# Performance work log

Measured on AMD Instinct MI355X. Metric: run time of the kernel, lower is better.

The kernel has to match this reference:

```python
import jax, jax.numpy as jnp
import numpy as np

B, S, D = 4, 2048, 1024

def setup_inputs() -> dict:
    key = jax.random.key(0)
    k1, k2, k3, k4 = jax.random.split(key, 4)
    scale = 1.0 / np.sqrt(D)
    x = jax.random.normal(k1, (B, S, D), dtype=jnp.float32)
    Wq = jax.random.normal(k2, (D, D), dtype=jnp.float32) * scale
    Wk = jax.random.normal(k3, (D, D), dtype=jnp.float32) * scale
    Wv = jax.random.normal(k4, (D, D), dtype=jnp.float32) * scale
    return {"x": x, "Wq": Wq, "Wk": Wk, "Wv": Wv}

def reference(x, Wq, Wk, Wv):
    # Linear projections (nn.Linear with bias=False computes x @ W.T)
    q = jnp.einsum('bsd,ed->bse', x, Wq)
    k = jnp.einsum('bsd,ed->bse', x, Wk)
    v = jnp.einsum('bsd,ed->bse', x, Wv)
    # HRR binding: circular convolution of k and v == elementwise product in FFT domain
    fq = jnp.fft.fft(q, axis=-1)
    fk = jnp.fft.fft(k, axis=-1)
    fv = jnp.fft.fft(v, axis=-1)
    # Causal associative memory: cumulative sum of bound key-value pairs over sequence
    mem = jnp.cumsum(fk * fv, axis=-2)  # [B, S, D] complex
    # Unbind with query via approximate inverse (complex conjugate of fft(q))
    out = jnp.fft.ifft(mem * jnp.conj(fq), axis=-1).real
    return out.astype(x.dtype)
```

## Files before the change

### kernel.cpp

```cpp
#include <hip/hip_runtime.h>

#define BB 4
#define SS 2048
#define DD 1024
#define MM 8192
#define CH 64
#define RR 32
#define PI_F 3.14159265358979323846f

typedef __attribute__((ext_vector_type(8))) short bf16x8;
typedef __attribute__((ext_vector_type(4))) float f32x4;

__device__ __forceinline__ unsigned short f2bf(float f) {
  unsigned int u = __float_as_uint(f);
  u = (u + 0x7FFFu + ((u >> 16) & 1u)) >> 16;
  return (unsigned short)u;
}
__device__ __forceinline__ float bf2f(unsigned short h) {
  return __uint_as_float(((unsigned int)h) << 16);
}

__global__ __launch_bounds__(256) void convert_bf16(
    const float* __restrict__ src, unsigned short* __restrict__ dst) {
  const long i = ((long)blockIdx.x * 256 + threadIdx.x) * 4;
  const float4 v = *(const float4*)&src[i];
  ushort4 o;
  o.x = f2bf(v.x); o.y = f2bf(v.y); o.z = f2bf(v.z); o.w = f2bf(v.w);
  *(ushort4*)&dst[i] = o;
}

__global__ __launch_bounds__(256) void convert_w(
    const float* __restrict__ Wq, const float* __restrict__ Wk,
    const float* __restrict__ Wv, unsigned short* __restrict__ dst) {
  const int z = blockIdx.y;
  const float* src = (z == 0) ? Wq : (z == 1) ? Wk : Wv;
  const long i = ((long)blockIdx.x * 256 + threadIdx.x) * 4;
  const float4 v = *(const float4*)&src[i];
  ushort4 o;
  o.x = f2bf(v.x); o.y = f2bf(v.y); o.z = f2bf(v.z); o.w = f2bf(v.w);
  *(ushort4*)&dst[(size_t)z * DD * DD + i] = o;
}

__device__ __forceinline__ void async16(const void* g, void* l) {
  __builtin_amdgcn_global_load_lds(
      (const __attribute__((address_space(1))) void*)g,
      (__attribute__((address_space(3))) void*)l, 16, 0, 0);
}

#define GW(n)  asm volatile("s_waitcnt vmcnt(" #n ")" ::: "memory")
#define BAR()  asm volatile("s_barrier" ::: "memory")
#define SB0()  __builtin_amdgcn_sched_barrier(0)

#define STA(buf, i, T) async16(xb + (size_t)(m0 + 32 * (i)) * DD + (T) * 64 + sOff, \
                               &Als[(buf) * 8192 + (i) * 2048 + slot8])
#define STB(buf, i, T) async16(W + (size_t)(n0 + 32 * (i)) * DD + (T) * 64 + sOff, \
                               &Bls[(buf) * 8192 + (i) * 2048 + slot8])
#define LDA(buf) { _Pragma("unroll") for (int mt = 0; mt < 4; ++mt) { \
    af[mt][0] = *(const bf16x8*)&Als[(buf) * 8192 + aRd + mt * 1024 + qoff0]; \
    af[mt][1] = *(const bf16x8*)&Als[(buf) * 8192 + aRd + mt * 1024 + qoff1]; } }
#define LDB(buf, nt, bank) { \
    bank[0] = *(const bf16x8*)&Bls[(buf) * 8192 + bRd + (nt) * 1024 + qoff0]; \
    bank[1] = *(const bf16x8*)&Bls[(buf) * 8192 + bRd + (nt) * 1024 + qoff1]; }
#define MMA(nt, bank) { __builtin_amdgcn_s_setprio(1); \
    _Pragma("unroll") for (int mt = 0; mt < 4; ++mt) { \
      acc[mt][nt] = __builtin_amdgcn_mfma_f32_16x16x32_bf16(af[mt][0], bank[0], acc[mt][nt], 0, 0, 0); \
      acc[mt][nt] = __builtin_amdgcn_mfma_f32_16x16x32_bf16(af[mt][1], bank[1], acc[mt][nt], 0, 0, 0); } \
    __builtin_amdgcn_s_setprio(0); }

__global__ __launch_bounds__(256, 2) void gemm_mfma(
    const unsigned short* __restrict__ xb,
    const unsigned short* __restrict__ Wb,
    float* __restrict__ outq, unsigned short* __restrict__ KV) {
  const int z = blockIdx.z;
  const unsigned short* W = Wb + (size_t)z * DD * DD;

  __shared__ unsigned short Als[2 * 8192];
  __shared__ unsigned short Bls[2 * 8192];

  const int tid  = threadIdx.x;
  const int lane = tid & 63;
  const int w    = tid >> 6;
  const int wm   = w >> 1;
  const int wn   = w & 1;
  const int fr   = lane & 15;
  const int kq   = lane >> 4;

  const int m0 = blockIdx.x * 128;
  const int n0 = blockIdx.y * 128;

  const int srow  = tid >> 3;
  const int sq    = (tid & 7) ^ (srow & 7);
  const int slot8 = tid * 8;
  const size_t sOff = (size_t)srow * DD + sq * 8;

  const int qoff0 = ((0 + kq) ^ (fr & 7)) * 8;
  const int qoff1 = ((4 + kq) ^ (fr & 7)) * 8;
  const int aRd = wm * 4096 + fr * 64;
  const int bRd = wn * 4096 + fr * 64;

  f32x4 acc[4][4] = {};
  bf16x8 af[4][2];
  bf16x8 bva[2], bvb[2];

  STA(0, 0, 0); STA(0, 1, 0); STA(0, 2, 0); STA(0, 3, 0);
  STB(0, 0, 0); STB(0, 1, 0); STB(0, 2, 0); STB(0, 3, 0);
  STA(1, 0, 1); STA(1, 1, 1); STA(1, 2, 1); STA(1, 3, 1);

  for (int T = 0; T < 14; ++T) {
    const int buf = T & 1;
    SB0(); GW(4); BAR();
    LDB(buf, 0, bva);
    LDA(buf);
    LDB(buf, 1, bvb);
    STB(buf ^ 1, 0, T + 1); STB(buf ^ 1, 1, T + 1);
    STB(buf ^ 1, 2, T + 1); STB(buf ^ 1, 3, T + 1);
    MMA(0, bva);
    MMA(1, bvb);
    SB0(); BAR();
    LDB(buf, 2, bva);
    LDB(buf, 3, bvb);
    STA(buf, 0, T + 2); STA(buf, 1, T + 2);
    STA(buf, 2, T + 2); STA(buf, 3, T + 2);
    MMA(2, bva);
    MMA(3, bvb);
  }
  SB0(); GW(4); BAR();
  LDB(0, 0, bva); LDA(0); LDB(0, 1, bvb);
  STB(1, 0, 15); STB(1, 1, 15); STB(1, 2, 15); STB(1, 3, 15);
  MMA(0, bva); MMA(1, bvb);
  SB0(); BAR();
  LDB(0, 2, bva); LDB(0, 3, bvb);
  MMA(2, bva); MMA(3, bvb);
  SB0(); GW(0); BAR();
  LDB(1, 0, bva); LDA(1); LDB(1, 1, bvb);
  MMA(0, bva); MMA(1, bvb);
  SB0(); BAR();
  LDB(1, 2, bva); LDB(1, 3, bvb);
  MMA(2, bva); MMA(3, bvb);

  const int col = lane & 15;
  const int r0  = (lane >> 4) * 4;
  const int mBase = m0 + wm * 64;
  const int nBase = n0 + wn * 64;
  if (z == 0) {
    #pragma unroll
    for (int mt = 0; mt < 4; ++mt)
      #pragma unroll
      for (int nt = 0; nt < 4; ++nt)
        #pragma unroll
        for (int r = 0; r < 4; ++r)
          outq[(size_t)(mBase + mt * 16 + r0 + r) * DD + nBase + nt * 16 + col] =
              acc[mt][nt][r];
  } else {
    unsigned short* Ck = KV + (size_t)(z - 1) * DD;
    #pragma unroll
    for (int mt = 0; mt < 4; ++mt)
      #pragma unroll
      for (int nt = 0; nt < 4; ++nt)
        #pragma unroll
        for (int r = 0; r < 4; ++r)
          Ck[(size_t)(mBase + mt * 16 + r0 + r) * 2048 + nBase + nt * 16 + col] =
              f2bf(acc[mt][nt][r]);
  }
}

__device__ __forceinline__ int pidx(int i) { return i + (i >> 6); }
#define BUFSZ 1040
__device__ __forceinline__ int pidx16(int i) { return i + (i >> 4); }
#define MEMSZ 546

__device__ __forceinline__ int rev4(int p) {
  unsigned r = __brev((unsigned)p) >> 22;
  return (int)(((r & 0x155u) << 1) | ((r & 0x2AAu) >> 1));
}

__host__ __device__ constexpr int clog2(int s) {
  return (s == 256) ? 8 : (s == 64) ? 6 : (s == 16) ? 4 : (s == 4) ? 2 : 0;
}

__device__ __forceinline__ void bf4(float2& a, float2& b, float2& c, float2& d,
                                    float c1, float s1) {
  const float c2 = c1 * c1 - s1 * s1, s2 = 2.0f * c1 * s1;
  const float c3 = c1 * c2 - s1 * s2, s3 = c1 * s2 + s1 * c2;
  const float Ar = a.x + c.x, Ai = a.y + c.y;
  const float Br = b.x + d.x, Bi = b.y + d.y;
  const float Cr = a.x - c.x, Ci = a.y - c.y;
  const float dr = b.x - d.x, di = b.y - d.y;
  const float y1r = Cr + di, y1i = Ci - dr;
  const float y2r = Ar - Br, y2i = Ai - Bi;
  const float y3r = Cr - di, y3i = Ci + dr;
  a = make_float2(Ar + Br, Ai + Bi);
  b = make_float2(y1r * c1 - y1i * s1, y1r * s1 + y1i * c1);
  c = make_float2(y2r * c2 - y2i * s2, y2r * s2 + y2i * c2);
  d = make_float2(y3r * c3 - y3i * s3, y3r * s3 + y3i * c3);
}

template <int S>
__device__ __forceinline__ void fwd_stage(float2 x[4], int t) {
  float c1 = 1.0f, s1 = 0.0f;
  if (S > 1) {
    const int j = t & (S - 1);
    __sincosf(-2.0f * PI_F * (float)j / (float)(4 * S), &s1, &c1);
  }
  bf4(x[0], x[1], x[2], x[3], c1, s1);
}

template <int S>
__device__ __forceinline__ void inv_stage(float2 x[4], int t) {
  float c1 = 1.0f, s1 = 0.0f;
  if (S > 1) {
    const int j = t & (S - 1);
    __sincosf(2.0f * PI_F * (float)j / (float)(4 * S), &s1, &c1);
  }
  const float c2 = c1 * c1 - s1 * s1, s2 = 2.0f * c1 * s1;
  const float c3 = c1 * c2 - s1 * s2, s3 = c1 * s2 + s1 * c2;
  const float u0r = x[0].x,                   u0i = x[0].y;
  const float u1r = x[1].x * c1 - x[1].y * s1, u1i = x[1].x * s1 + x[1].y * c1;
  const float u2r = x[2].x * c2 - x[2].y * s2, u2i = x[2].x * s2 + x[2].y * c2;
  const float u3r = x[3].x * c3 - x[3].y * s3, u3i = x[3].x * s3 + x[3].y * c3;
  const float Er = u0r + u2r, Ei = u0i + u2i;
  const float Fr = u0r - u2r, Fi = u0i - u2i;
  const float Gr = u1r + u3r, Gi = u1i + u3i;
  const float Hr = u1r - u3r, Hi = u1i - u3i;
  x[0] = make_float2(Er + Gr, Ei + Gi);
  x[1] = make_float2(Fr - Hi, Fi + Hr);
  x[2] = make_float2(Er - Gr, Ei - Gi);
  x[3] = make_float2(Fr + Hi, Fi - Hr);
}

template <int SW, int SR>
__device__ __forceinline__ void xchg(float2* buf, float2 x[4], int t) {
  constexpr int LW2 = clog2(SW), LR = clog2(SR);
  #pragma unroll
  for (int n = 0; n < 4; ++n)
    buf[pidx(((t >> LW2) << (LW2 + 2)) + (t & (SW - 1)) + n * SW)] = x[n];
  __syncthreads();
  #pragma unroll
  for (int n = 0; n < 4; ++n)
    x[n] = buf[pidx(((t >> LR) << (LR + 2)) + (t & (SR - 1)) + n * SR)];
  __syncthreads();
}

__device__ __forceinline__ void fwd_fft(float2* buf, float2 x[4], int t) {
  fwd_stage<256>(x, t); xchg<256, 64>(buf, x, t);
  fwd_stage<64>(x, t);  xchg<64, 16>(buf, x, t);
  fwd_stage<16>(x, t);  xchg<16, 4>(buf, x, t);
  fwd_stage<4>(x, t);   xchg<4, 1>(buf, x, t);
  fwd_stage<1>(x, t);
  #pragma unroll
  for (int n = 0; n < 4; ++n) buf[pidx(4 * t + n)] = x[n];
  __syncthreads();
}

#define LKW() asm volatile("s_waitcnt lgkmcnt(0)" ::: "memory")

__global__ __launch_bounds__(256) void bind_kernel(unsigned short* __restrict__ KV) {
  __shared__ float2 rbufs[4][BUFSZ];
  const int l  = threadIdx.x & 63;
  const int wv = threadIdx.x >> 6;
  float2* rbuf = rbufs[wv];
  unsigned short* row = KV + ((long)blockIdx.x * 4 + wv) * 2048;

  float2 x[16];
  #pragma unroll
  for (int j = 0; j < 16; ++j) {
    const int n = l + 64 * j;
    x[j] = make_float2(bf2f(row[n]), bf2f(row[1024 + n]));
  }

  #pragma unroll
  for (int b = 0; b < 4; ++b) {
    float s1, c1;
    __sincosf(-2.0f * PI_F * (float)(l + 64 * b) / 1024.0f, &s1, &c1);
    bf4(x[b], x[b + 4], x[b + 8], x[b + 12], c1, s1);
  }
  {
    float s1, c1;
    __sincosf(-2.0f * PI_F * (float)l / 256.0f, &s1, &c1);
    #pragma unroll
    for (int b = 0; b < 4; ++b)
      bf4(x[4 * b], x[4 * b + 1], x[4 * b + 2], x[4 * b + 3], c1, s1);
  }

  #pragma unroll
  for (int j = 0; j < 16; ++j)
    rbuf[(l ^ ((j & 3) << 2)) + 64 * j] = x[j];
  LKW();
  const int g = l >> 2, cc = l & 3;
  #pragma unroll
  for (int j = 0; j < 16; ++j) {
    const int q = 64 * g + cc + 4 * j;
    x[j] = rbuf[q ^ (((q >> 6) & 3) << 2)];
  }

  #pragma unroll
  for (int b = 0; b < 4; ++b) {
    float s1, c1;
    __sincosf(-2.0f * PI_F * (float)(cc + 4 * b) / 64.0f, &s1, &c1);
    bf4(x[b], x[b + 4], x[b + 8], x[b + 12], c1, s1);
  }
  {
    float s1, c1;
    __sincosf(-2.0f * PI_F * (float)cc / 16.0f, &s1, &c1);
    #pragma unroll
    for (int b = 0; b < 4; ++b)
      bf4(x[4 * b], x[4 * b + 1], x[4 * b + 2], x[4 * b + 3], c1, s1);
  }

  #pragma unroll
  for (int j = 0; j < 16; ++j) {
    const int q = 64 * g + cc + 4 * j;
    rbuf[q ^ ((q >> 4) & 15)] = x[j];
  }
  LKW();
  #pragma unroll
  for (int i = 0; i < 16; ++i) {
    const int q = 16 * l + i;
    x[i] = rbuf[q ^ ((q >> 4) & 15)];
  }

  #pragma unroll
  for (int b = 0; b < 4; ++b)
    bf4(x[4 * b], x[4 * b + 1], x[4 * b + 2], x[4 * b + 3], 1.0f, 0.0f);

  #pragma unroll
  for (int i = 0; i < 16; ++i)
    rbuf[pidx(16 * l + i)] = x[i];
  LKW();

  float2* Prow = (float2*)row;
  #pragma unroll
  for (int m = 0; m < 8; ++m) {
    const int s = l + 64 * m;
    if (s == 0) {
      const float2 W0   = rbuf[pidx(0)];
      const float2 W512 = rbuf[pidx(2)];
      Prow[0] = make_float2(W0.x * W0.y, W512.x * W512.y);
    } else {
      const int p1 = rev4(s);
      const int p2 = rev4(1024 - s);
      const float2 F1 = rbuf[pidx(p1)], F2 = rbuf[pidx(p2)];
      const float fkr = 0.5f * (F1.x + F2.x), fki = 0.5f * (F1.y - F2.y);
      const float fvr = 0.5f * (F1.y + F2.y), fvi = 0.5f * (F2.x - F1.x);
      Prow[s] = make_float2(fkr * fvr - fki * fvi, fkr * fvi + fki * fvr);
    }
  }
}

__global__ __launch_bounds__(256) void scan_chunk_sum(
    const float2* __restrict__ P, float2* __restrict__ csum) {
  const int chunk = blockIdx.x;
  const int batch = blockIdx.y >> 1;
  const int f = (blockIdx.y & 1) * 256 + threadIdx.x;
  long base = ((long)batch * SS + (long)chunk * RR) * 512 + f;
  float sr = 0.0f, si = 0.0f;
  #pragma unroll
  for (int i0 = 0; i0 < RR; i0 += 8) {
    float2 p[8];
    #pragma unroll
    for (int j = 0; j < 8; ++j) p[j] = P[base + (long)(i0 + j) * 512];
    #pragma unroll
    for (int j = 0; j < 8; ++j) { sr += p[j].x; si += p[j].y; }
  }
  csum[((long)batch * CH + chunk) * 512 + f] = make_float2(sr, si);
}

__global__ __launch_bounds__(256) void scan_chunk_scan(float2* csum) {
  const int col   = blockIdx.x * 4 + (threadIdx.x >> 6);
  const int batch = col >> 9;
  const int f     = col & 511;
  const int c     = threadIdx.x & 63;
  const long idx  = ((long)batch * CH + c) * 512 + f;
  const float2 v  = csum[idx];
  float rr = v.x, ri = v.y;
  #pragma unroll
  for (int d = 1; d < 64; d <<= 1) {
    const float ox = __shfl_up(rr, d);
    const float oy = __shfl_up(ri, d);
    if (c >= d) { rr += ox; ri += oy; }
  }
  float ex = __shfl_up(rr, 1);
  float ey = __shfl_up(ri, 1);
  if (c == 0) { ex = 0.0f; ey = 0.0f; }
  csum[idx] = make_float2(ex, ey);
}

__global__ __launch_bounds__(256) void scan_apply(
    float2* __restrict__ P, const float2* __restrict__ csum) {
  const int chunk = blockIdx.x;
  const int batch = blockIdx.y >> 1;
  const int f = (blockIdx.y & 1) * 256 + threadIdx.x;
  float2 off = csum[((long)batch * CH + chunk) * 512 + f];
  float ar = off.x, ai = off.y;
  long base = ((long)batch * SS + (long)chunk * RR) * 512 + f;
  #pragma unroll
  for (int i0 = 0; i0 < RR; i0 += 8) {
    float2 p[8];
    #pragma unroll
    for (int j = 0; j < 8; ++j) p[j] = P[base + (long)(i0 + j) * 512];
    #pragma unroll
    for (int j = 0; j < 8; ++j) {
      ar += p[j].x; ai += p[j].y;
      P[base + (long)(i0 + j) * 512] = make_float2(ar, ai);
    }
  }
}

__global__ __launch_bounds__(256) void unbind_kernel(
    float* __restrict__ qout, const float2* __restrict__ mem) {
  __shared__ float2 buf[BUFSZ];
  __shared__ float2 m0s[MEMSZ], m1s[MEMSZ];
  const int t = threadIdx.x;
  const long r0 = (long)blockIdx.x * 2;
  float* row0 = qout + r0 * DD;
  float* row1 = row0 + DD;
  const float2* mem0 = mem + r0 * 512;
  const float2* mem1 = mem0 + 512;

  float2 x[4];
  #pragma unroll
  for (int n = 0; n < 4; ++n) {
    const int i = t + 256 * n;
    x[n] = make_float2(row0[i], row1[i]);
  }
  #pragma unroll
  for (int n = 0; n < 2; ++n) {
    const int s = t + 256 * n;
    const float2 a = mem0[s], b = mem1[s];
    if (s == 0) {
      m0s[pidx16(0)]   = make_float2(a.x, 0.0f);
      m0s[pidx16(512)] = make_float2(a.y, 0.0f);
      m1s[pidx16(0)]   = make_float2(b.x, 0.0f);
      m1s[pidx16(512)] = make_float2(b.y, 0.0f);
    } else {
      m0s[pidx16(s)] = a;
      m1s[pidx16(s)] = b;
    }
  }
  fwd_fft(buf, x, t);

  float2 z[4];
  #pragma unroll
  for (int m = 0; m < 4; ++m) {
    const int p   = t + 256 * m;
    const int bin = rev4(p);
    const int p2  = rev4((1024 - bin) & 1023);
    const float2 F1 = buf[pidx(p)], F2 = buf[pidx(p2)];
    const float q0r = 0.5f * (F1.x + F2.x), q0i = 0.5f * (F1.y - F2.y);
    const float q1r = 0.5f * (F1.y + F2.y), q1i = 0.5f * (F2.x - F1.x);
    const int  ix = (bin <= 512) ? bin : 1024 - bin;
    const float sg = (bin <= 512) ? 1.0f : -1.0f;
    float2 m0 = m0s[pidx16(ix)], m1 = m1s[pidx16(ix)];
    m0.y *= sg; m1.y *= sg;
    const float z0r = m0.x * q0r + m0.y * q0i, z0i = m0.y * q0r - m0.x * q0i;
    const float z1r = m1.x * q1r + m1.y * q1i, z1i = m1.y * q1r - m1.x * q1i;
    z[m] = make_float2(z0r - z1i, z0i + z1r);
  }
  __syncthreads();
  #pragma unroll
  for (int m = 0; m < 4; ++m) buf[pidx(t + 256 * m)] = z[m];
  __syncthreads();
  #pragma unroll
  for (int n = 0; n < 4; ++n) x[n] = buf[pidx(4 * t + n)];

  inv_stage<1>(x, t);   xchg<1, 4>(buf, x, t);
  inv_stage<4>(x, t);   xchg<4, 16>(buf, x, t);
  inv_stage<16>(x, t);  xchg<16, 64>(buf, x, t);
  inv_stage<64>(x, t);  xchg<64, 256>(buf, x, t);
  inv_stage<256>(x, t);

  const float sc = 1.0f / 1024.0f;
  #pragma unroll
  for (int n = 0; n < 4; ++n) {
    const int i = t + 256 * n;
    row0[i] = x[n].x * sc;
    row1[i] = x[n].y * sc;
  }
}

extern "C" void kernel_launch(void* const* d_in, const int* in_sizes, int n_in,
                              void* d_out, int out_size, void* d_ws, size_t ws_size,
                              hipStream_t stream) {
  (void)in_sizes; (void)n_in; (void)out_size;
  const float* x  = (const float*)d_in[0];
  const float* Wq = (const float*)d_in[1];
  const float* Wk = (const float*)d_in[2];
  const float* Wv = (const float*)d_in[3];
  float* out = (float*)d_out;

  const size_t wbytes = (size_t)3 * DD * DD * 2;
  auto need = [&](size_t MHr, size_t nB) {
    return wbytes + MHr * DD * 2 + MHr * 4096 + nB * CH * 512 * 8;
  };
  const int nPass = (ws_size >= need(8192, 4)) ? 1 : 2;
  const size_t MH = MM / nPass;
  const int    nB = BB / nPass;

  char* ws = (char*)d_ws;
  unsigned short* Wb = (unsigned short*)ws;
  unsigned short* xb = (unsigned short*)(ws + wbytes);
  unsigned short* KV = (unsigned short*)(ws + wbytes + MH * DD * 2);
  float2*       csum = (float2*)((char*)KV + MH * 4096);

  convert_w<<<dim3(DD * DD / 1024, 3), 256, 0, stream>>>(Wq, Wk, Wv, Wb);

  for (int h = 0; h < nPass; ++h) {
    const float* xh   = x   + (size_t)h * MH * DD;
    float*       outh = out + (size_t)h * MH * DD;

    convert_bf16<<<MH * DD / 1024, 256, 0, stream>>>(xh, xb);
    gemm_mfma<<<dim3(MH / 128, DD / 128, 3), dim3(256), 0, stream>>>(xb, Wb, outh, KV);
    bind_kernel<<<MH / 4, 256, 0, stream>>>(KV);
    scan_chunk_sum<<<dim3(CH, nB * 2), 256, 0, stream>>>((const float2*)KV, csum);
    scan_chunk_scan<<<nB * 128, 256, 0, stream>>>(csum);
    scan_apply<<<dim3(CH, nB * 2), 256, 0, stream>>>((float2*)KV, csum);
    unbind_kernel<<<MH / 2, 256, 0, stream>>>(outh, (const float2*)KV);
  }
}
```

Before: 220.6 us.

## Rewrite unbind kernel as per-wave radix-4 FFT without block barriers

The unbind kernel moves from one 256-thread block per row pair (radix-4 FFT with __syncthreads exchanges) to one wavefront per row pair, reusing the wave-local 16-element forward FFT from bind_kernel and adding a matching wave-local inverse FFT. Memory spectra are read directly from global memory instead of being staged in shared memory. The aim is to drop block-level barriers and shared staging. In exchange each thread uses more registers (16 complex values), and the global reads for the memory spectrum are scattered.

```diff
diff --git a/kernel.cpp b/kernel.cpp
--- a/kernel.cpp
+++ b/kernel.cpp
@@ -166,16 +166,10 @@
 
 __device__ __forceinline__ int pidx(int i) { return i + (i >> 6); }
 #define BUFSZ 1040
-__device__ __forceinline__ int pidx16(int i) { return i + (i >> 4); }
-#define MEMSZ 546
 
 __device__ __forceinline__ int rev4(int p) {
   unsigned r = __brev((unsigned)p) >> 22;
   return (int)(((r & 0x155u) << 1) | ((r & 0x2AAu) >> 1));
-}
-
-__host__ __device__ constexpr int clog2(int s) {
-  return (s == 256) ? 8 : (s == 64) ? 6 : (s == 16) ? 4 : (s == 4) ? 2 : 0;
 }
 
 __device__ __forceinline__ void bf4(float2& a, float2& b, float2& c, float2& d,
@@ -195,64 +189,82 @@
   d = make_float2(y3r * c3 - y3i * s3, y3r * s3 + y3i * c3);
 }
 
-template <int S>
-__device__ __forceinline__ void fwd_stage(float2 x[4], int t) {
-  float c1 = 1.0f, s1 = 0.0f;
-  if (S > 1) {
-    const int j = t & (S - 1);
-    __sincosf(-2.0f * PI_F * (float)j / (float)(4 * S), &s1, &c1);
-  }
-  bf4(x[0], x[1], x[2], x[3], c1, s1);
-}
-
-template <int S>
-__device__ __forceinline__ void inv_stage(float2 x[4], int t) {
-  float c1 = 1.0f, s1 = 0.0f;
-  if (S > 1) {
-    const int j = t & (S - 1);
-    __sincosf(2.0f * PI_F * (float)j / (float)(4 * S), &s1, &c1);
-  }
+__device__ __forceinline__ void ibf4(float2& a, float2& b, float2& c, float2& d,
+                                     float c1, float s1) {
   const float c2 = c1 * c1 - s1 * s1, s2 = 2.0f * c1 * s1;
   const float c3 = c1 * c2 - s1 * s2, s3 = c1 * s2 + s1 * c2;
-  const float u0r = x[0].x,                   u0i = x[0].y;
-  const float u1r = x[1].x * c1 - x[1].y * s1, u1i = x[1].x * s1 + x[1].y * c1;
-  const float u2r = x[2].x * c2 - x[2].y * s2, u2i = x[2].x * s2 + x[2].y * c2;
-  const float u3r = x[3].x * c3 - x[3].y * s3, u3i = x[3].x * s3 + x[3].y * c3;
+  const float u0r = a.x,                 u0i = a.y;
+  const float u1r = b.x * c1 - b.y * s1, u1i = b.x * s1 + b.y * c1;
+  const float u2r = c.x * c2 - c.y * s2, u2i = c.x * s2 + c.y * c2;
+  const float u3r = d.x * c3 - d.y * s3, u3i = d.x * s3 + d.y * c3;
   const float Er = u0r + u2r, Ei = u0i + u2i;
   const float Fr = u0r - u2r, Fi = u0i - u2i;
   const float Gr = u1r + u3r, Gi = u1i + u3i;
   const float Hr = u1r - u3r, Hi = u1i - u3i;
-  x[0] = make_float2(Er + Gr, Ei + Gi);
-  x[1] = make_float2(Fr - Hi, Fi + Hr);
-  x[2] = make_float2(Er - Gr, Ei - Gi);
-  x[3] = make_float2(Fr + Hi, Fi - Hr);
-}
-
-template <int SW, int SR>
-__device__ __forceinline__ void xchg(float2* buf, float2 x[4], int t) {
-  constexpr int LW2 = clog2(SW), LR = clog2(SR);
-  #pragma unroll
-  for (int n = 0; n < 4; ++n)
-    buf[pidx(((t >> LW2) << (LW2 + 2)) + (t & (SW - 1)) + n * SW)] = x[n];
-  __syncthreads();
-  #pragma unroll
-  for (int n = 0; n < 4; ++n)
-    x[n] = buf[pidx(((t >> LR) << (LR + 2)) + (t & (SR - 1)) + n * SR)];
-  __syncthreads();
-}
-
-__device__ __forceinline__ void fwd_fft(float2* buf, float2 x[4], int t) {
-  fwd_stage<256>(x, t); xchg<256, 64>(buf, x, t);
-  fwd_stage<64>(x, t);  xchg<64, 16>(buf, x, t);
-  fwd_stage<16>(x, t);  xchg<16, 4>(buf, x, t);
-  fwd_stage<4>(x, t);   xchg<4, 1>(buf, x, t);
-  fwd_stage<1>(x, t);
-  #pragma unroll
-  for (int n = 0; n < 4; ++n) buf[pidx(4 * t + n)] = x[n];
-  __syncthreads();
+  a = make_float2(Er + Gr, Ei + Gi);
+  b = make_float2(Fr - Hi, Fi + Hr);
+  c = make_float2(Er - Gr, Ei - Gi);
+  d = make_float2(Fr + Hi, Fi - Hr);
 }
 
 #define LKW() asm volatile("s_waitcnt lgkmcnt(0)" ::: "memory")
+
+__device__ __forceinline__ void wave_fwd_fft(float2* rbuf, float2 x[16], int l) {
+  #pragma unroll
+  for (int b = 0; b < 4; ++b) {
+    float s1, c1;
+    __sincosf(-2.0f * PI_F * (float)(l + 64 * b) / 1024.0f, &s1, &c1);
+    bf4(x[b], x[b + 4], x[b + 8], x[b + 12], c1, s1);
+  }
+  {
+    float s1, c1;
+    __sincosf(-2.0f * PI_F * (float)l / 256.0f, &s1, &c1);
+    #pragma unroll
+    for (int b = 0; b < 4; ++b)
+      bf4(x[4 * b], x[4 * b + 1], x[4 * b + 2], x[4 * b + 3], c1, s1);
+  }
+  #pragma unroll
+  for (int j = 0; j < 16; ++j)
+    rbuf[(l ^ ((j & 3) << 2)) + 64 * j] = x[j];
+  LKW();
+  const int g = l >> 2, cc = l & 3;
+  #pragma unroll
+  for (int j = 0; j < 16; ++j) {
+    const int q = 64 * g + cc + 4 * j;
+    x[j] = rbuf[q ^ (((q >> 6) & 3) << 2)];
+  }
+  #pragma unroll
+  for (int b = 0; b < 4; ++b) {
+    float s1, c1;
+    __sincosf(-2.0f * PI_F * (float)(cc + 4 * b) / 64.0f, &s1, &c1);
+    bf4(x[b], x[b + 4], x[b + 8], x[b + 12], c1, s1);
+  }
+  {
+    float s1, c1;
+    __sincosf(-2.0f * PI_F * (float)cc / 16.0f, &s1, &c1);
+    #pragma unroll
+    for (int b = 0; b < 4; ++b)
+      bf4(x[4 * b], x[4 * b + 1], x[4 * b + 2], x[4 * b + 3], c1, s1);
+  }
+  #pragma unroll
+  for (int j = 0; j < 16; ++j) {
+    const int q = 64 * g + cc + 4 * j;
+    rbuf[q ^ ((q >> 4) & 15)] = x[j];
+  }
+  LKW();
+  #pragma unroll
+  for (int i = 0; i < 16; ++i) {
+    const int q = 16 * l + i;
+    x[i] = rbuf[q ^ ((q >> 4) & 15)];
+  }
+  #pragma unroll
+  for (int b = 0; b < 4; ++b)
+    bf4(x[4 * b], x[4 * b + 1], x[4 * b + 2], x[4 * b + 3], 1.0f, 0.0f);
+  #pragma unroll
+  for (int i = 0; i < 16; ++i)
+    rbuf[pidx(16 * l + i)] = x[i];
+  LKW();
+}
 
 __global__ __launch_bounds__(256) void bind_kernel(unsigned short* __restrict__ KV) {
   __shared__ float2 rbufs[4][BUFSZ];
@@ -267,66 +279,7 @@
     const int n = l + 64 * j;
     x[j] = make_float2(bf2f(row[n]), bf2f(row[1024 + n]));
   }
-
-  #pragma unroll
-  for (int b = 0; b < 4; ++b) {
-    float s1, c1;
-    __sincosf(-2.0f * PI_F * (float)(l + 64 * b) / 1024.0f, &s1, &c1);
-    bf4(x[b], x[b + 4], x[b + 8], x[b + 12], c1, s1);
-  }
-  {
-    float s1, c1;
-    __sincosf(-2.0f * PI_F * (float)l / 256.0f, &s1, &c1);
-    #pragma unroll
-    for (int b = 0; b < 4; ++b)
-      bf4(x[4 * b], x[4 * b + 1], x[4 * b + 2], x[4 * b + 3], c1, s1);
-  }
-
-  #pragma unroll
-  for (int j = 0; j < 16; ++j)
-    rbuf[(l ^ ((j & 3) << 2)) + 64 * j] = x[j];
-  LKW();
-  const int g = l >> 2, cc = l & 3;
-  #pragma unroll
-  for (int j = 0; j < 16; ++j) {
-    const int q = 64 * g + cc + 4 * j;
-    x[j] = rbuf[q ^ (((q >> 6) & 3) << 2)];
-  }
-
-  #pragma unroll
-  for (int b = 0; b < 4; ++b) {
-    float s1, c1;
-    __sincosf(-2.0f * PI_F * (float)(cc + 4 * b) / 64.0f, &s1, &c1);
-    bf4(x[b], x[b + 4], x[b + 8], x[b + 12], c1, s1);
-  }
-  {
-    float s1, c1;
-    __sincosf(-2.0f * PI_F * (float)cc / 16.0f, &s1, &c1);
-    #pragma unroll
-    for (int b = 0; b < 4; ++b)
-      bf4(x[4 * b], x[4 * b + 1], x[4 * b + 2], x[4 * b + 3], c1, s1);
-  }
-
-  #pragma unroll
-  for (int j = 0; j < 16; ++j) {
-    const int q = 64 * g + cc + 4 * j;
-    rbuf[q ^ ((q >> 4) & 15)] = x[j];
-  }
-  LKW();
-  #pragma unroll
-  for (int i = 0; i < 16; ++i) {
-    const int q = 16 * l + i;
-    x[i] = rbuf[q ^ ((q >> 4) & 15)];
-  }
-
-  #pragma unroll
-  for (int b = 0; b < 4; ++b)
-    bf4(x[4 * b], x[4 * b + 1], x[4 * b + 2], x[4 * b + 3], 1.0f, 0.0f);
-
-  #pragma unroll
-  for (int i = 0; i < 16; ++i)
-    rbuf[pidx(16 * l + i)] = x[i];
-  LKW();
+  wave_fwd_fft(rbuf, x, l);
 
   float2* Prow = (float2*)row;
   #pragma unroll
@@ -408,73 +361,111 @@
 
 __global__ __launch_bounds__(256) void unbind_kernel(
     float* __restrict__ qout, const float2* __restrict__ mem) {
-  __shared__ float2 buf[BUFSZ];
-  __shared__ float2 m0s[MEMSZ], m1s[MEMSZ];
-  const int t = threadIdx.x;
-  const long r0 = (long)blockIdx.x * 2;
+  __shared__ float2 rbufs[4][BUFSZ];
+  const int l  = threadIdx.x & 63;
+  const int wv = threadIdx.x >> 6;
+  float2* rbuf = rbufs[wv];
+  const long r0 = ((long)blockIdx.x * 4 + wv) * 2;
   float* row0 = qout + r0 * DD;
   float* row1 = row0 + DD;
   const float2* mem0 = mem + r0 * 512;
   const float2* mem1 = mem0 + 512;
 
-  float2 x[4];
-  #pragma unroll
-  for (int n = 0; n < 4; ++n) {
-    const int i = t + 256 * n;
-    x[n] = make_float2(row0[i], row1[i]);
-  }
-  #pragma unroll
-  for (int n = 0; n < 2; ++n) {
-    const int s = t + 256 * n;
-    const float2 a = mem0[s], b = mem1[s];
-    if (s == 0) {
-      m0s[pidx16(0)]   = make_float2(a.x, 0.0f);
-      m0s[pidx16(512)] = make_float2(a.y, 0.0f);
-      m1s[pidx16(0)]   = make_float2(b.x, 0.0f);
-      m1s[pidx16(512)] = make_float2(b.y, 0.0f);
-    } else {
-      m0s[pidx16(s)] = a;
-      m1s[pidx16(s)] = b;
-    }
-  }
-  fwd_fft(buf, x, t);
-
-  float2 z[4];
-  #pragma unroll
-  for (int m = 0; m < 4; ++m) {
-    const int p   = t + 256 * m;
+  float2 x[16];
+  #pragma unroll
+  for (int j = 0; j < 16; ++j) {
+    const int n = l + 64 * j;
+    x[j] = make_float2(row0[n], row1[n]);
+  }
+  wave_fwd_fft(rbuf, x, l);
+
+  #pragma unroll
+  for (int i = 0; i < 16; ++i) {
+    const int p   = 16 * l + i;
     const int bin = rev4(p);
     const int p2  = rev4((1024 - bin) & 1023);
-    const float2 F1 = buf[pidx(p)], F2 = buf[pidx(p2)];
+    const float2 F1 = rbuf[pidx(p)], F2 = rbuf[pidx(p2)];
     const float q0r = 0.5f * (F1.x + F2.x), q0i = 0.5f * (F1.y - F2.y);
     const float q1r = 0.5f * (F1.y + F2.y), q1i = 0.5f * (F2.x - F1.x);
-    const int  ix = (bin <= 512) ? bin : 1024 - bin;
+    const int   ix = (bin <= 512) ? bin : 1024 - bin;
     const float sg = (bin <= 512) ? 1.0f : -1.0f;
-    float2 m0 = m0s[pidx16(ix)], m1 = m1s[pidx16(ix)];
-    m0.y *= sg; m1.y *= sg;
+    float2 m0, m1;
+    if (ix == 0) {
+      m0 = make_float2(mem0[0].x, 0.0f); m1 = make_float2(mem1[0].x, 0.0f);
+    } else if (ix == 512) {
+      m0 = make_float2(mem0[0].y, 0.0f); m1 = make_float2(mem1[0].y, 0.0f);
+    } else {
+      m0 = mem0[ix]; m1 = mem1[ix];
+      m0.y *= sg; m1.y *= sg;
+    }
     const float z0r = m0.x * q0r + m0.y * q0i, z0i = m0.y * q0r - m0.x * q0i;
     const float z1r = m1.x * q1r + m1.y * q1i, z1i = m1.y * q1r - m1.x * q1i;
-    z[m] = make_float2(z0r - z1i, z0i + z1r);
-  }
-  __syncthreads();
-  #pragma unroll
-  for (int m = 0; m < 4; ++m) buf[pidx(t + 256 * m)] = z[m];
-  __syncthreads();
-  #pragma unroll
-  for (int n = 0; n < 4; ++n) x[n] = buf[pidx(4 * t + n)];
-
-  inv_stage<1>(x, t);   xchg<1, 4>(buf, x, t);
-  inv_stage<4>(x, t);   xchg<4, 16>(buf, x, t);
-  inv_stage<16>(x, t);  xchg<16, 64>(buf, x, t);
-  inv_stage<64>(x, t);  xchg<64, 256>(buf, x, t);
-  inv_stage<256>(x, t);
+    x[i] = make_float2(z0r - z1i, z0i + z1r);
+  }
+
+  #pragma unroll
+  for (int b = 0; b < 4; ++b)
+    ibf4(x[4 * b], x[4 * b + 1], x[4 * b + 2], x[4 * b + 3], 1.0f, 0.0f);
+
+  #pragma unroll
+  for (int i = 0; i < 16; ++i) {
+    const int q = 16 * l + i;
+    rbuf[q ^ ((q >> 4) & 15)] = x[i];
+  }
+  LKW();
+  const int g = l >> 2, cc = l & 3;
+  #pragma unroll
+  for (int j = 0; j < 16; ++j) {
+    const int q = 64 * g + cc + 4 * j;
+    x[j] = rbuf[q ^ ((q >> 4) & 15)];
+  }
+
+  {
+    float s1, c1;
+    __sincosf(2.0f * PI_F * (float)cc / 16.0f, &s1, &c1);
+    #pragma unroll
+    for (int b = 0; b < 4; ++b)
+      ibf4(x[4 * b], x[4 * b + 1], x[4 * b + 2], x[4 * b + 3], c1, s1);
+  }
+  #pragma unroll
+  for (int b = 0; b < 4; ++b) {
+    float s1, c1;
+    __sincosf(2.0f * PI_F * (float)(cc + 4 * b) / 64.0f, &s1, &c1);
+    ibf4(x[b], x[b + 4], x[b + 8], x[b + 12], c1, s1);
+  }
+
+  #pragma unroll
+  for (int j = 0; j < 16; ++j) {
+    const int q = 64 * g + cc + 4 * j;
+    rbuf[q ^ (((q >> 6) & 3) << 2)] = x[j];
+  }
+  LKW();
+  #pragma unroll
+  for (int j = 0; j < 16; ++j) {
+    const int q = l + 64 * j;
+    x[j] = rbuf[q ^ (((q >> 6) & 3) << 2)];
+  }
+
+  {
+    float s1, c1;
+    __sincosf(2.0f * PI_F * (float)l / 256.0f, &s1, &c1);
+    #pragma unroll
+    for (int b = 0; b < 4; ++b)
+      ibf4(x[4 * b], x[4 * b + 1], x[4 * b + 2], x[4 * b + 3], c1, s1);
+  }
+  #pragma unroll
+  for (int c2 = 0; c2 < 4; ++c2) {
+    float s1, c1;
+    __sincosf(2.0f * PI_F * (float)(l + 64 * c2) / 1024.0f, &s1, &c1);
+    ibf4(x[c2], x[c2 + 4], x[c2 + 8], x[c2 + 12], c1, s1);
+  }
 
   const float sc = 1.0f / 1024.0f;
   #pragma unroll
-  for (int n = 0; n < 4; ++n) {
-    const int i = t + 256 * n;
-    row0[i] = x[n].x * sc;
-    row1[i] = x[n].y * sc;
+  for (int j = 0; j < 16; ++j) {
+    const int n = l + 64 * j;
+    row0[n] = x[j].x * sc;
+    row1[n] = x[j].y * sc;
   }
 }
 
@@ -514,6 +505,6 @@
     scan_chunk_sum<<<dim3(CH, nB * 2), 256, 0, stream>>>((const float2*)KV, csum);
     scan_chunk_scan<<<nB * 128, 256, 0, stream>>>(csum);
     scan_apply<<<dim3(CH, nB * 2), 256, 0, stream>>>((float2*)KV, csum);
-    unbind_kernel<<<MH / 2, 256, 0, stream>>>(outh, (const float2*)KV);
-  }
-}
+    unbind_kernel<<<MH / 8, 256, 0, stream>>>(outh, (const float2*)KV);
+  }
+}
```

Result: no change. 219.7 us (-0.4%).
